# Performance work log

Hardware: AMD Instinct MI355X
Metric: run time of the kernel (lower is better)

The kernel has to match this reference:

```python
import jax, jax.numpy as jnp
import numpy as np

N = 100000      # num_nodes
FEAT = 256      # num_features
H = 128         # hidden
C = 40          # num_classes
K = 4           # hops
RWS = 10        # random-walk samples per node
NL = 2          # nlayer
ALPHA = 0.1


def setup_inputs() -> dict:
    key = jax.random.key(0)
    ks = jax.random.split(key, 10)
    x = jax.random.normal(ks[0], (N, FEAT), dtype=jnp.float32)
    degree = jax.random.uniform(ks[1], (N,), minval=1.0, maxval=64.0, dtype=jnp.float32)
    # precomputed random-walk endpoints per layer per hop: [NL, K, N*RWS]
    ends = jax.random.randint(ks[2], (NL, K, N * RWS), 0, N, dtype=jnp.int32)
    # att init: alpha*(1-alpha)^k, last entry (1-alpha)^K, tiled per layer
    a = ALPHA * (1.0 - ALPHA) ** jnp.arange(K + 1, dtype=jnp.float32)
    a = a.at[-1].set((1.0 - ALPHA) ** K)
    att = jnp.tile(a[None, :], (NL, 1))
    def lin(k, fan_in, fan_out):
        s = 1.0 / np.sqrt(fan_in)
        return jax.random.uniform(k, (fan_in, fan_out), minval=-s, maxval=s, dtype=jnp.float32)
    W0 = lin(ks[3], FEAT, H)
    b0 = jnp.zeros((H,), dtype=jnp.float32)
    W1 = lin(ks[4], H, H)
    b1 = jnp.zeros((H,), dtype=jnp.float32)
    W2 = lin(ks[5], H, C)
    b2 = jnp.zeros((C,), dtype=jnp.float32)
    return {"x": x, "degree": degree, "ends": ends, "att": att,
            "W0": W0, "b0": b0, "W1": W1, "b1": b1, "W2": W2, "b2": b2}


def reference(x, degree, ends, att, W0, b0, W1, b1, W2, b2):
    Ws = [(W0, b0), (W1, b1)]
    starts = jnp.repeat(jnp.arange(N), RWS)          # [N*RWS] walk start node ids
    d_sqrt = jnp.sqrt(degree)                        # degree^0.5
    d_isqrt = jax.lax.rsqrt(degree)                  # degree^-0.5
    h = x
    for i in range(NL):
        W, b = Ws[i]
        h = h @ W + b                                # Linear (dropout p=0)
        mask = att[i]                                # [K+1]
        agg = h * mask[0]
        for k in range(1, K + 1):
            e = ends[i, k - 1]                       # [N*RWS] hop-k endpoints
            w = d_sqrt[starts] * d_isqrt[e]          # degree reweighting
            samp = (w[:, None] * h[e]).reshape(N, RWS, h.shape[1]).mean(axis=1)
            agg = agg + samp * mask[k]
        h = jax.nn.relu(agg)
    logits = h @ W2 + b2
    return jax.nn.log_softmax(logits, axis=1)
```

## Files before the change

kernel.cpp:

```cpp
#include <hip/hip_runtime.h>
#include <math.h>

#define NNODES 100000
#define NFEAT  256
#define HID    128
#define NCLS   40
#define KHOP   4
#define RWSAMP 10
#define KP1    5

typedef __bf16 bf16;
typedef __attribute__((ext_vector_type(8)))  __bf16 bf16x8;
typedef __attribute__((ext_vector_type(2)))  float  f32x2;
typedef __attribute__((ext_vector_type(16))) float  f32x16;

__global__ __launch_bounds__(256) void prep_w(
    const float* __restrict__ W0, const float* __restrict__ W1,
    const float* __restrict__ W2,
    bf16* __restrict__ Wt0, bf16* __restrict__ Wt1, bf16* __restrict__ Wt2)
{
    int tid = blockIdx.x * 256 + threadIdx.x;
    if (tid < 128 * 256) {
        int n = tid >> 8, k = tid & 255;
        Wt0[tid] = (bf16)W0[k * 128 + n];
    } else if (tid < 128 * 256 + 128 * 128) {
        int i = tid - 128 * 256;
        int n = i >> 7, k = i & 127;
        Wt1[i] = (bf16)W1[k * 128 + n];
    } else if (tid < 128 * 256 + 128 * 128 + 64 * 128) {
        int i = tid - (128 * 256 + 128 * 128);
        int n = i >> 7, k = i & 127;
        Wt2[i] = (n < NCLS) ? (bf16)W2[k * NCLS + n] : (bf16)0.0f;
    }
}

template<int K, bool A_BF16>
__global__ __launch_bounds__(256) void gemm_nodes(
    const void* __restrict__ Av, const bf16* __restrict__ Wt,
    const float* __restrict__ bias, unsigned char* __restrict__ F8, int M)
{
    constexpr int BK  = 128;
    constexpr int LDB = BK + 4;
    __shared__ bf16 Bs[128 * LDB];
    __shared__ bf16 As[4][32 * LDB];

    const int tid  = threadIdx.x;
    const int wv   = tid >> 6;
    const int lane = tid & 63;
    const int l31  = lane & 31;
    const int lhi  = lane >> 5;
    const int blockRow = blockIdx.x * 128;
    const int rowBase  = blockRow + wv * 32;

    const bf16*  Ab = (const bf16*)Av;
    const float* Af = (const float*)Av;

    f32x16 acc[4];
#pragma unroll
    for (int t = 0; t < 4; ++t)
#pragma unroll
        for (int r = 0; r < 16; ++r) acc[t][r] = 0.0f;

    for (int k0 = 0; k0 < K; k0 += BK) {
        if (k0) __syncthreads();
#pragma unroll 4
        for (int l = 0; l < 8; ++l) {
            int c   = tid + l * 256;
            int row = c >> 4;
            int kc  = (c & 15) * 8;
            uint4 v = *(const uint4*)(Wt + (size_t)row * K + k0 + kc);
            *(uint2*)&Bs[row * LDB + kc]     = make_uint2(v.x, v.y);
            *(uint2*)&Bs[row * LDB + kc + 4] = make_uint2(v.z, v.w);
        }
        __syncthreads();

        if (A_BF16) {
#pragma unroll 4
            for (int l = 0; l < 8; ++l) {
                int c  = lane + l * 64;
                int r  = c >> 4;
                int kc = (c & 15) * 8;
                int gr = min(rowBase + r, M - 1);
                uint4 v = *(const uint4*)(Ab + (size_t)gr * K + k0 + kc);
                *(uint2*)&As[wv][r * LDB + kc]     = make_uint2(v.x, v.y);
                *(uint2*)&As[wv][r * LDB + kc + 4] = make_uint2(v.z, v.w);
            }
        } else {
#pragma unroll 4
            for (int l = 0; l < 16; ++l) {
                int c  = lane + l * 64;
                int r  = c >> 5;
                int kc = (c & 31) * 4;
                int gr = min(rowBase + r, M - 1);
                float4 v = *(const float4*)(Af + (size_t)gr * K + k0 + kc);
                union { bf16 h[4]; uint2 u; } t4;
                t4.h[0] = (bf16)v.x; t4.h[1] = (bf16)v.y;
                t4.h[2] = (bf16)v.z; t4.h[3] = (bf16)v.w;
                *(uint2*)&As[wv][r * LDB + kc] = t4.u;
            }
        }

#pragma unroll
        for (int ks = 0; ks < BK / 16; ++ks) {
            const int ko = ks * 16 + lhi * 8;
            union { uint2 u2[2]; bf16x8 v; } ua, ub;
            ua.u2[0] = *(const uint2*)&As[wv][l31 * LDB + ko];
            ua.u2[1] = *(const uint2*)&As[wv][l31 * LDB + ko + 4];
            bf16x8 a = ua.v;
#pragma unroll
            for (int t = 0; t < 4; ++t) {
                ub.u2[0] = *(const uint2*)&Bs[(t * 32 + l31) * LDB + ko];
                ub.u2[1] = *(const uint2*)&Bs[(t * 32 + l31) * LDB + ko + 4];
                acc[t] = __builtin_amdgcn_mfma_f32_32x32x16_bf16(a, ub.v, acc[t], 0, 0, 0);
            }
        }
    }

    __syncthreads();
    unsigned* ldsq = (unsigned*)Bs;

#pragma unroll
    for (int t = 0; t < 4; ++t) {
        int col = t * 32 + l31;
        float bc = bias[col];
#pragma unroll
        for (int G = 0; G < 4; ++G) {
            float v0 = acc[t][4 * G + 0] + bc;
            float v1 = acc[t][4 * G + 1] + bc;
            float v2 = acc[t][4 * G + 2] + bc;
            float v3 = acc[t][4 * G + 3] + bc;
            int p = __builtin_amdgcn_cvt_pk_fp8_f32(v0, v1, 0, false);
            p = __builtin_amdgcn_cvt_pk_fp8_f32(v2, v3, p, true);
            ldsq[(wv * 8 + 2 * G + lhi) * 128 + col] = (unsigned)p;
        }
    }
    __syncthreads();

    {
        const int j  = tid & 31;
        const int Q0 = (tid >> 5) * 4;
#pragma unroll
        for (int qq = 0; qq < 4; ++qq) {
            int Q = Q0 + qq;
            uint4 d = *(const uint4*)&ldsq[Q * 128 + 4 * j];
            int growb = blockRow + 4 * Q;
#pragma unroll
            for (int i = 0; i < 4; ++i) {
                unsigned sel = ((unsigned)(4 + i) << 8) | (unsigned)i;
                unsigned lo = __builtin_amdgcn_perm(d.y, d.x, sel);
                unsigned hi = __builtin_amdgcn_perm(d.w, d.z, sel);
                unsigned o  = __builtin_amdgcn_perm(hi, lo, 0x05040100u);
                if (growb + i < M)
                    *(unsigned*)(F8 + (size_t)(growb + i) * 128 + 4 * j) = o;
            }
        }
    }
}

__global__ __launch_bounds__(256) void agg_relu_fp8(
    const unsigned char* __restrict__ hf8, bf16* __restrict__ hout,
    const int* __restrict__ ends, const float* __restrict__ degree,
    const float* __restrict__ att)
{
    __shared__ int2 sew[4][2][40];

    const int wv   = threadIdx.x >> 6;
    const int lane = threadIdx.x & 63;
    const int n0   = blockIdx.x * 8 + wv * 2;

    for (int en = lane; en < 80; en += 64) {
        int which = en >= 40;
        int l = en - which * 40;
        int n = n0 + which;
        int k = l / RWSAMP, s = l - k * RWSAMP;
        int e = ends[(size_t)k * (NNODES * RWSAMP) + (size_t)n * RWSAMP + s];
        float w = att[k + 1] * (1.0f / RWSAMP) * sqrtf(degree[n]) * rsqrtf(degree[e]);
        sew[wv][which][l] = make_int2(e << 7, __float_as_int(w));
    }

    const int q  = lane >> 4;
    const int c8 = (lane & 15) * 8;

    f32x2 a0[4], a1[4];
#pragma unroll
    for (int i = 0; i < 4; ++i) { a0[i] = (f32x2){0.f, 0.f}; a1[i] = (f32x2){0.f, 0.f}; }

#pragma unroll
    for (int t = 0; t < 10; ++t) {
        int2 ew0 = sew[wv][0][4 * t + q];
        int2 ew1 = sew[wv][1][4 * t + q];
        uint2 g0 = *(const uint2*)(hf8 + (unsigned)ew0.x + (unsigned)c8);
        uint2 g1 = *(const uint2*)(hf8 + (unsigned)ew1.x + (unsigned)c8);
        float w0 = __int_as_float(ew0.y);
        float w1 = __int_as_float(ew1.y);
        f32x2 w20 = {w0, w0}, w21 = {w1, w1};
        a0[0] = __builtin_elementwise_fma(w20, __builtin_amdgcn_cvt_pk_f32_fp8((int)g0.x, false), a0[0]);
        a0[1] = __builtin_elementwise_fma(w20, __builtin_amdgcn_cvt_pk_f32_fp8((int)g0.x, true),  a0[1]);
        a0[2] = __builtin_elementwise_fma(w20, __builtin_amdgcn_cvt_pk_f32_fp8((int)g0.y, false), a0[2]);
        a0[3] = __builtin_elementwise_fma(w20, __builtin_amdgcn_cvt_pk_f32_fp8((int)g0.y, true),  a0[3]);
        a1[0] = __builtin_elementwise_fma(w21, __builtin_amdgcn_cvt_pk_f32_fp8((int)g1.x, false), a1[0]);
        a1[1] = __builtin_elementwise_fma(w21, __builtin_amdgcn_cvt_pk_f32_fp8((int)g1.x, true),  a1[1]);
        a1[2] = __builtin_elementwise_fma(w21, __builtin_amdgcn_cvt_pk_f32_fp8((int)g1.y, false), a1[2]);
        a1[3] = __builtin_elementwise_fma(w21, __builtin_amdgcn_cvt_pk_f32_fp8((int)g1.y, true),  a1[3]);
    }

#pragma unroll
    for (int i = 0; i < 4; ++i) {
        a0[i].x += __shfl_xor(a0[i].x, 16, 64); a0[i].y += __shfl_xor(a0[i].y, 16, 64);
        a1[i].x += __shfl_xor(a1[i].x, 16, 64); a1[i].y += __shfl_xor(a1[i].y, 16, 64);
        a0[i].x += __shfl_xor(a0[i].x, 32, 64); a0[i].y += __shfl_xor(a0[i].y, 32, 64);
        a1[i].x += __shfl_xor(a1[i].x, 32, 64); a1[i].y += __shfl_xor(a1[i].y, 32, 64);
    }

    if (q < 2) {
        const int n = n0 + q;
        f32x2* a = (q == 0) ? a0 : a1;
        const float att0 = att[0];
        f32x2 av = {att0, att0};
        unsigned vs = ((unsigned)n << 7) + (unsigned)c8;
        uint2 sv = *(const uint2*)(hf8 + vs);
        a[0] = __builtin_elementwise_fma(av, __builtin_amdgcn_cvt_pk_f32_fp8((int)sv.x, false), a[0]);
        a[1] = __builtin_elementwise_fma(av, __builtin_amdgcn_cvt_pk_f32_fp8((int)sv.x, true),  a[1]);
        a[2] = __builtin_elementwise_fma(av, __builtin_amdgcn_cvt_pk_f32_fp8((int)sv.y, false), a[2]);
        a[3] = __builtin_elementwise_fma(av, __builtin_amdgcn_cvt_pk_f32_fp8((int)sv.y, true),  a[3]);

        f32x2 z = {0.f, 0.f};
#pragma unroll
        for (int i = 0; i < 4; ++i) a[i] = __builtin_elementwise_max(a[i], z);

        union { bf16 h[8]; uint4 u; } st;
        st.h[0] = (bf16)a[0].x; st.h[1] = (bf16)a[0].y;
        st.h[2] = (bf16)a[1].x; st.h[3] = (bf16)a[1].y;
        st.h[4] = (bf16)a[2].x; st.h[5] = (bf16)a[2].y;
        st.h[6] = (bf16)a[3].x; st.h[7] = (bf16)a[3].y;
        *(uint4*)(hout + (size_t)n * HID + c8) = st.u;
    }
}

__global__ __launch_bounds__(256) void head_mfma(
    const bf16* __restrict__ h, const bf16* __restrict__ Wt2,
    const float* __restrict__ b2, float* __restrict__ out, int M)
{
    constexpr int K = HID, LDB = K + 8;
    __shared__ bf16 Bs[64 * LDB];

    const int tid = threadIdx.x;
    constexpr int CPR = K / 8;
    for (int f = tid; f < 64 * CPR; f += 256) {
        int row = f / CPR;
        int kc  = (f % CPR) * 8;
        *(uint4*)&Bs[row * LDB + kc] = *(const uint4*)(Wt2 + (size_t)row * K + kc);
    }
    __syncthreads();

    const int wv   = tid >> 6;
    const int lane = tid & 63;
    const int l31  = lane & 31;
    const int lhi  = lane >> 5;
    const int blockRow = blockIdx.x * 128;
    const int arow = min(blockRow + wv * 32 + l31, M - 1);

    f32x16 acc[2];
#pragma unroll
    for (int t = 0; t < 2; ++t)
#pragma unroll
        for (int r = 0; r < 16; ++r) acc[t][r] = 0.0f;

#pragma unroll
    for (int ks = 0; ks < K / 16; ++ks) {
        bf16x8 a = *(const bf16x8*)(h + (size_t)arow * K + ks * 16 + lhi * 8);
#pragma unroll
        for (int t = 0; t < 2; ++t) {
            bf16x8 b = *(const bf16x8*)&Bs[(t * 32 + l31) * LDB + ks * 16 + lhi * 8];
            acc[t] = __builtin_amdgcn_mfma_f32_32x32x16_bf16(a, b, acc[t], 0, 0, 0);
        }
    }

    const float bc0 = b2[l31];
    const float bc1 = (l31 < 8) ? b2[32 + l31] : 0.0f;

#pragma unroll
    for (int r = 0; r < 16; ++r) {
        float v0 = acc[0][r] + bc0;
        float v1 = (l31 < 8) ? (acc[1][r] + bc1) : -INFINITY;

        float m = fmaxf(v0, v1);
#pragma unroll
        for (int off = 16; off > 0; off >>= 1)
            m = fmaxf(m, __shfl_xor(m, off, 64));

        float s = __expf(v0 - m) + ((l31 < 8) ? __expf(v1 - m) : 0.0f);
#pragma unroll
        for (int off = 16; off > 0; off >>= 1)
            s += __shfl_xor(s, off, 64);

        float ls = __logf(s);
        int grow = blockRow + wv * 32 + (r & 3) + 8 * (r >> 2) + 4 * lhi;
        if (grow < M) {
            out[(size_t)grow * NCLS + l31] = v0 - m - ls;
            if (l31 < 8)
                out[(size_t)grow * NCLS + 32 + l31] = v1 - m - ls;
        }
    }
}

extern "C" void kernel_launch(void* const* d_in, const int* in_sizes, int n_in,
                              void* d_out, int out_size, void* d_ws, size_t ws_size,
                              hipStream_t stream)
{
    const float* x      = (const float*)d_in[0];
    const float* degree = (const float*)d_in[1];
    const int*   ends   = (const int*)  d_in[2];
    const float* att    = (const float*)d_in[3];
    const float* W0     = (const float*)d_in[4];
    const float* b0     = (const float*)d_in[5];
    const float* W1     = (const float*)d_in[6];
    const float* b1     = (const float*)d_in[7];
    const float* W2     = (const float*)d_in[8];
    const float* b2     = (const float*)d_in[9];
    float* out = (float*)d_out;

    bf16* hb0 = (bf16*)d_ws;
    bf16* hb1 = hb0 + (size_t)NNODES * HID;
    unsigned char* hf8 = (unsigned char*)(hb1 + (size_t)NNODES * HID);
    bf16* Wt0 = (bf16*)(hf8 + (size_t)NNODES * HID);
    bf16* Wt1 = Wt0 + 128 * 256;
    bf16* Wt2 = Wt1 + 128 * 128;

    const int prepN = 128 * 256 + 128 * 128 + 64 * 128;
    prep_w<<<(prepN + 255) / 256, 256, 0, stream>>>(W0, W1, W2, Wt0, Wt1, Wt2);

    const int gGemm = (NNODES + 127) / 128;
    const int gAgg  = (NNODES + 7) / 8;

    gemm_nodes<NFEAT, false><<<gGemm, 256, 0, stream>>>(x, Wt0, b0, hf8, NNODES);
    agg_relu_fp8<<<gAgg, 256, 0, stream>>>(hf8, hb1, ends, degree, att);
    gemm_nodes<HID, true><<<gGemm, 256, 0, stream>>>(hb1, Wt1, b1, hf8, NNODES);
    agg_relu_fp8<<<gAgg, 256, 0, stream>>>(
        hf8, hb0, ends + (size_t)KHOP * NNODES * RWSAMP, degree, att + KP1);
    head_mfma<<<gGemm, 256, 0, stream>>>(hb0, Wt2, b2, out, NNODES);
}
```

Baseline: 350.6 us.

## Stage gathered fp8 neighbor rows into LDS via global_load_lds before aggregation

The aggregation kernel now issues all 82 row gathers per wave (40 walk endpoints per node plus the self row, for two nodes) as direct global-to-LDS loads into a per-wave staging buffer, waits once, then reads the rows from LDS for the FMA reduction. Endpoint offsets and weights are split into separate LDS arrays, and the self term is folded into the same staged rows. The intent is to expose more gathers in flight at once and to avoid register-held global loads. In exchange it uses about 42KB of LDS per block, which may reduce occupancy. It also adds a full vmcnt wait with no overlap between loading and compute.

```diff
diff --git a/kernel.cpp b/kernel.cpp
--- a/kernel.cpp
+++ b/kernel.cpp
@@ -13,6 +13,9 @@
 typedef __attribute__((ext_vector_type(8)))  __bf16 bf16x8;
 typedef __attribute__((ext_vector_type(2)))  float  f32x2;
 typedef __attribute__((ext_vector_type(16))) float  f32x16;
+
+typedef __attribute__((address_space(3))) unsigned       lds_u32;
+typedef __attribute__((address_space(1))) const unsigned glb_u32;
 
 __global__ __launch_bounds__(256) void prep_w(
     const float* __restrict__ W0, const float* __restrict__ W1,
@@ -162,21 +165,46 @@
     const int* __restrict__ ends, const float* __restrict__ degree,
     const float* __restrict__ att)
 {
-    __shared__ int2 sew[4][2][40];
+    __shared__ __attribute__((aligned(16))) unsigned char stage[4][82 * 128];
+    __shared__ int   sewE[4][82];
+    __shared__ float sewW[4][82];
 
     const int wv   = threadIdx.x >> 6;
     const int lane = threadIdx.x & 63;
     const int n0   = blockIdx.x * 8 + wv * 2;
 
-    for (int en = lane; en < 80; en += 64) {
-        int which = en >= 40;
-        int l = en - which * 40;
-        int n = n0 + which;
-        int k = l / RWSAMP, s = l - k * RWSAMP;
-        int e = ends[(size_t)k * (NNODES * RWSAMP) + (size_t)n * RWSAMP + s];
-        float w = att[k + 1] * (1.0f / RWSAMP) * sqrtf(degree[n]) * rsqrtf(degree[e]);
-        sew[wv][which][l] = make_int2(e << 7, __float_as_int(w));
-    }
+    for (int en = lane; en < 82; en += 64) {
+        int node = en > 40;
+        int j = en - node * 41;
+        int n = n0 + node;
+        int e;
+        float w;
+        if (j == 40) {
+            e = n;
+            w = att[0];
+        } else {
+            int k = j / RWSAMP, s = j - k * RWSAMP;
+            e = ends[(size_t)k * (NNODES * RWSAMP) + (size_t)n * RWSAMP + s];
+            w = att[k + 1] * (1.0f / RWSAMP) * sqrtf(degree[n]) * rsqrtf(degree[e]);
+        }
+        sewE[wv][en] = e << 7;
+        sewW[wv][en] = w;
+    }
+
+    {
+        const unsigned char* gbase = hf8 + (unsigned)((lane & 31) * 4);
+#pragma unroll
+        for (int t = 0; t < 41; ++t) {
+            int r = 2 * t + (lane >> 5);
+            int eoff = sewE[wv][r];
+            __builtin_amdgcn_global_load_lds(
+                (glb_u32*)(gbase + (unsigned)eoff),
+                (lds_u32*)&stage[wv][t * 256],
+                4, 0, 0);
+        }
+    }
+    asm volatile("s_waitcnt vmcnt(0)" ::: "memory");
+    __builtin_amdgcn_sched_barrier(0);
 
     const int q  = lane >> 4;
     const int c8 = (lane & 15) * 8;
@@ -187,12 +215,11 @@
 
 #pragma unroll
     for (int t = 0; t < 10; ++t) {
-        int2 ew0 = sew[wv][0][4 * t + q];
-        int2 ew1 = sew[wv][1][4 * t + q];
-        uint2 g0 = *(const uint2*)(hf8 + (unsigned)ew0.x + (unsigned)c8);
-        uint2 g1 = *(const uint2*)(hf8 + (unsigned)ew1.x + (unsigned)c8);
-        float w0 = __int_as_float(ew0.y);
-        float w1 = __int_as_float(ew1.y);
+        int j = 4 * t + q;
+        uint2 g0 = *(const uint2*)&stage[wv][j * 128 + c8];
+        uint2 g1 = *(const uint2*)&stage[wv][(41 + j) * 128 + c8];
+        float w0 = sewW[wv][j];
+        float w1 = sewW[wv][41 + j];
         f32x2 w20 = {w0, w0}, w21 = {w1, w1};
         a0[0] = __builtin_elementwise_fma(w20, __builtin_amdgcn_cvt_pk_f32_fp8((int)g0.x, false), a0[0]);
         a0[1] = __builtin_elementwise_fma(w20, __builtin_amdgcn_cvt_pk_f32_fp8((int)g0.x, true),  a0[1]);
@@ -215,10 +242,10 @@
     if (q < 2) {
         const int n = n0 + q;
         f32x2* a = (q == 0) ? a0 : a1;
-        const float att0 = att[0];
+        const int selfRow = q ? 81 : 40;
+        uint2 sv = *(const uint2*)&stage[wv][selfRow * 128 + c8];
+        float att0 = sewW[wv][selfRow];
         f32x2 av = {att0, att0};
-        unsigned vs = ((unsigned)n << 7) + (unsigned)c8;
-        uint2 sv = *(const uint2*)(hf8 + vs);
         a[0] = __builtin_elementwise_fma(av, __builtin_amdgcn_cvt_pk_f32_fp8((int)sv.x, false), a[0]);
         a[1] = __builtin_elementwise_fma(av, __builtin_amdgcn_cvt_pk_f32_fp8((int)sv.x, true),  a[1]);
         a[2] = __builtin_elementwise_fma(av, __builtin_amdgcn_cvt_pk_f32_fp8((int)sv.y, false), a[2]);
```

Result: slower. 393.9 us (+12.4%).

## Fold degree scaling into GEMM epilogue and restructure aggregation to one node per wave

Applied to the files above, without the earlier changes.

The GEMM epilogue now multiplies each row by rsqrt(degree) before FP8 quantisation. The aggregation therefore no longer gathers degree[e] for every random-walk endpoint and applies sqrt(degree[n]) once, after ReLU. The aggregation kernel is also rebuilt so each wave handles one node with 16-byte gathers, 8 lanes per row and a one-step software prefetch. The self term is handled as a 41st sample slot. Pre-scaling values before FP8 changes their dynamic range, which may affect quantisation error slightly.

```diff
diff --git a/kernel.cpp b/kernel.cpp
--- a/kernel.cpp
+++ b/kernel.cpp
@@ -37,7 +37,8 @@
 template<int K, bool A_BF16>
 __global__ __launch_bounds__(256) void gemm_nodes(
     const void* __restrict__ Av, const bf16* __restrict__ Wt,
-    const float* __restrict__ bias, unsigned char* __restrict__ F8, int M)
+    const float* __restrict__ bias, const float* __restrict__ degree,
+    unsigned char* __restrict__ F8, int M)
 {
     constexpr int BK  = 128;
     constexpr int LDB = BK + 4;
@@ -116,6 +117,15 @@
         }
     }
 
+    float rsd[16];
+#pragma unroll
+    for (int G = 0; G < 4; ++G) {
+        int r0 = blockRow + 4 * (wv * 8 + 2 * G + lhi);
+#pragma unroll
+        for (int c = 0; c < 4; ++c)
+            rsd[4 * G + c] = rsqrtf(degree[min(r0 + c, M - 1)]);
+    }
+
     __syncthreads();
     unsigned* ldsq = (unsigned*)Bs;
 
@@ -125,10 +135,10 @@
         float bc = bias[col];
 #pragma unroll
         for (int G = 0; G < 4; ++G) {
-            float v0 = acc[t][4 * G + 0] + bc;
-            float v1 = acc[t][4 * G + 1] + bc;
-            float v2 = acc[t][4 * G + 2] + bc;
-            float v3 = acc[t][4 * G + 3] + bc;
+            float v0 = (acc[t][4 * G + 0] + bc) * rsd[4 * G + 0];
+            float v1 = (acc[t][4 * G + 1] + bc) * rsd[4 * G + 1];
+            float v2 = (acc[t][4 * G + 2] + bc) * rsd[4 * G + 2];
+            float v3 = (acc[t][4 * G + 3] + bc) * rsd[4 * G + 3];
             int p = __builtin_amdgcn_cvt_pk_fp8_f32(v0, v1, 0, false);
             p = __builtin_amdgcn_cvt_pk_fp8_f32(v2, v3, p, true);
             ldsq[(wv * 8 + 2 * G + lhi) * 128 + col] = (unsigned)p;
@@ -162,78 +172,88 @@
     const int* __restrict__ ends, const float* __restrict__ degree,
     const float* __restrict__ att)
 {
-    __shared__ int2 sew[4][2][40];
+    __shared__ int   sewE[4][48];
+    __shared__ float sewW[4][48];
 
     const int wv   = threadIdx.x >> 6;
     const int lane = threadIdx.x & 63;
-    const int n0   = blockIdx.x * 8 + wv * 2;
-
-    for (int en = lane; en < 80; en += 64) {
-        int which = en >= 40;
-        int l = en - which * 40;
-        int n = n0 + which;
-        int k = l / RWSAMP, s = l - k * RWSAMP;
-        int e = ends[(size_t)k * (NNODES * RWSAMP) + (size_t)n * RWSAMP + s];
-        float w = att[k + 1] * (1.0f / RWSAMP) * sqrtf(degree[n]) * rsqrtf(degree[e]);
-        sew[wv][which][l] = make_int2(e << 7, __float_as_int(w));
-    }
-
-    const int q  = lane >> 4;
-    const int c8 = (lane & 15) * 8;
-
-    f32x2 a0[4], a1[4];
-#pragma unroll
-    for (int i = 0; i < 4; ++i) { a0[i] = (f32x2){0.f, 0.f}; a1[i] = (f32x2){0.f, 0.f}; }
-
-#pragma unroll
-    for (int t = 0; t < 10; ++t) {
-        int2 ew0 = sew[wv][0][4 * t + q];
-        int2 ew1 = sew[wv][1][4 * t + q];
-        uint2 g0 = *(const uint2*)(hf8 + (unsigned)ew0.x + (unsigned)c8);
-        uint2 g1 = *(const uint2*)(hf8 + (unsigned)ew1.x + (unsigned)c8);
-        float w0 = __int_as_float(ew0.y);
-        float w1 = __int_as_float(ew1.y);
-        f32x2 w20 = {w0, w0}, w21 = {w1, w1};
-        a0[0] = __builtin_elementwise_fma(w20, __builtin_amdgcn_cvt_pk_f32_fp8((int)g0.x, false), a0[0]);
-        a0[1] = __builtin_elementwise_fma(w20, __builtin_amdgcn_cvt_pk_f32_fp8((int)g0.x, true),  a0[1]);
-        a0[2] = __builtin_elementwise_fma(w20, __builtin_amdgcn_cvt_pk_f32_fp8((int)g0.y, false), a0[2]);
-        a0[3] = __builtin_elementwise_fma(w20, __builtin_amdgcn_cvt_pk_f32_fp8((int)g0.y, true),  a0[3]);
-        a1[0] = __builtin_elementwise_fma(w21, __builtin_amdgcn_cvt_pk_f32_fp8((int)g1.x, false), a1[0]);
-        a1[1] = __builtin_elementwise_fma(w21, __builtin_amdgcn_cvt_pk_f32_fp8((int)g1.x, true),  a1[1]);
-        a1[2] = __builtin_elementwise_fma(w21, __builtin_amdgcn_cvt_pk_f32_fp8((int)g1.y, false), a1[2]);
-        a1[3] = __builtin_elementwise_fma(w21, __builtin_amdgcn_cvt_pk_f32_fp8((int)g1.y, true),  a1[3]);
-    }
-
-#pragma unroll
-    for (int i = 0; i < 4; ++i) {
-        a0[i].x += __shfl_xor(a0[i].x, 16, 64); a0[i].y += __shfl_xor(a0[i].y, 16, 64);
-        a1[i].x += __shfl_xor(a1[i].x, 16, 64); a1[i].y += __shfl_xor(a1[i].y, 16, 64);
-        a0[i].x += __shfl_xor(a0[i].x, 32, 64); a0[i].y += __shfl_xor(a0[i].y, 32, 64);
-        a1[i].x += __shfl_xor(a1[i].x, 32, 64); a1[i].y += __shfl_xor(a1[i].y, 32, 64);
-    }
-
-    if (q < 2) {
-        const int n = n0 + q;
-        f32x2* a = (q == 0) ? a0 : a1;
-        const float att0 = att[0];
-        f32x2 av = {att0, att0};
-        unsigned vs = ((unsigned)n << 7) + (unsigned)c8;
-        uint2 sv = *(const uint2*)(hf8 + vs);
-        a[0] = __builtin_elementwise_fma(av, __builtin_amdgcn_cvt_pk_f32_fp8((int)sv.x, false), a[0]);
-        a[1] = __builtin_elementwise_fma(av, __builtin_amdgcn_cvt_pk_f32_fp8((int)sv.x, true),  a[1]);
-        a[2] = __builtin_elementwise_fma(av, __builtin_amdgcn_cvt_pk_f32_fp8((int)sv.y, false), a[2]);
-        a[3] = __builtin_elementwise_fma(av, __builtin_amdgcn_cvt_pk_f32_fp8((int)sv.y, true),  a[3]);
-
-        f32x2 z = {0.f, 0.f};
-#pragma unroll
-        for (int i = 0; i < 4; ++i) a[i] = __builtin_elementwise_max(a[i], z);
-
-        union { bf16 h[8]; uint4 u; } st;
-        st.h[0] = (bf16)a[0].x; st.h[1] = (bf16)a[0].y;
-        st.h[2] = (bf16)a[1].x; st.h[3] = (bf16)a[1].y;
-        st.h[4] = (bf16)a[2].x; st.h[5] = (bf16)a[2].y;
-        st.h[6] = (bf16)a[3].x; st.h[7] = (bf16)a[3].y;
-        *(uint4*)(hout + (size_t)n * HID + c8) = st.u;
+    const int n    = blockIdx.x * 4 + wv;
+
+    if (lane < 48) {
+        int j = lane;
+        int e; float w;
+        if (j < 40) {
+            int k = j / RWSAMP, ss = j - k * RWSAMP;
+            e = ends[(size_t)k * (NNODES * RWSAMP) + (size_t)n * RWSAMP + ss];
+            w = att[k + 1] * (1.0f / RWSAMP);
+        } else if (j == 40) { e = n; w = att[0]; }
+        else                { e = n; w = 0.0f;  }
+        sewE[wv][j] = e << 7;
+        sewW[wv][j] = w;
+    }
+
+    const int s  = lane >> 3;
+    const int fc = lane & 7;
+
+    int   eoff[6];
+    float wt[6];
+#pragma unroll
+    for (int t = 0; t < 6; ++t) {
+        eoff[t] = sewE[wv][8 * t + s];
+        wt[t]   = sewW[wv][8 * t + s];
+    }
+
+    const unsigned char* base = hf8 + (unsigned)(fc * 16);
+    uint4 cur = *(const uint4*)(base + (unsigned)eoff[0]);
+
+    f32x2 acc[8];
+#pragma unroll
+    for (int i = 0; i < 8; ++i) acc[i] = (f32x2){0.f, 0.f};
+
+#pragma unroll
+    for (int t = 0; t < 6; ++t) {
+        uint4 nxt = cur;
+        if (t < 5) nxt = *(const uint4*)(base + (unsigned)eoff[t + 1]);
+        float w = wt[t];
+        f32x2 w2 = {w, w};
+        acc[0] = __builtin_elementwise_fma(w2, __builtin_amdgcn_cvt_pk_f32_fp8((int)cur.x, false), acc[0]);
+        acc[1] = __builtin_elementwise_fma(w2, __builtin_amdgcn_cvt_pk_f32_fp8((int)cur.x, true),  acc[1]);
+        acc[2] = __builtin_elementwise_fma(w2, __builtin_amdgcn_cvt_pk_f32_fp8((int)cur.y, false), acc[2]);
+        acc[3] = __builtin_elementwise_fma(w2, __builtin_amdgcn_cvt_pk_f32_fp8((int)cur.y, true),  acc[3]);
+        acc[4] = __builtin_elementwise_fma(w2, __builtin_amdgcn_cvt_pk_f32_fp8((int)cur.z, false), acc[4]);
+        acc[5] = __builtin_elementwise_fma(w2, __builtin_amdgcn_cvt_pk_f32_fp8((int)cur.z, true),  acc[5]);
+        acc[6] = __builtin_elementwise_fma(w2, __builtin_amdgcn_cvt_pk_f32_fp8((int)cur.w, false), acc[6]);
+        acc[7] = __builtin_elementwise_fma(w2, __builtin_amdgcn_cvt_pk_f32_fp8((int)cur.w, true),  acc[7]);
+        cur = nxt;
+    }
+
+#pragma unroll
+    for (int i = 0; i < 8; ++i) {
+        acc[i].x += __shfl_xor(acc[i].x, 8, 64);  acc[i].y += __shfl_xor(acc[i].y, 8, 64);
+        acc[i].x += __shfl_xor(acc[i].x, 16, 64); acc[i].y += __shfl_xor(acc[i].y, 16, 64);
+        acc[i].x += __shfl_xor(acc[i].x, 32, 64); acc[i].y += __shfl_xor(acc[i].y, 32, 64);
+    }
+
+    if (s == 0) {
+        float sd = sqrtf(degree[n]);
+        f32x2 sd2 = {sd, sd}, z = {0.f, 0.f};
+#pragma unroll
+        for (int i = 0; i < 8; ++i) {
+            acc[i] = __builtin_elementwise_max(acc[i], z);
+            acc[i] = acc[i] * sd2;
+        }
+        union { bf16 h[8]; uint4 u; } lo, hi;
+        lo.h[0] = (bf16)acc[0].x; lo.h[1] = (bf16)acc[0].y;
+        lo.h[2] = (bf16)acc[1].x; lo.h[3] = (bf16)acc[1].y;
+        lo.h[4] = (bf16)acc[2].x; lo.h[5] = (bf16)acc[2].y;
+        lo.h[6] = (bf16)acc[3].x; lo.h[7] = (bf16)acc[3].y;
+        hi.h[0] = (bf16)acc[4].x; hi.h[1] = (bf16)acc[4].y;
+        hi.h[2] = (bf16)acc[5].x; hi.h[3] = (bf16)acc[5].y;
+        hi.h[4] = (bf16)acc[6].x; hi.h[5] = (bf16)acc[6].y;
+        hi.h[6] = (bf16)acc[7].x; hi.h[7] = (bf16)acc[7].y;
+        bf16* orow = hout + (size_t)n * HID + fc * 16;
+        *(uint4*)orow       = lo.u;
+        *(uint4*)(orow + 8) = hi.u;
     }
 }
 
@@ -331,11 +351,11 @@
     prep_w<<<(prepN + 255) / 256, 256, 0, stream>>>(W0, W1, W2, Wt0, Wt1, Wt2);
 
     const int gGemm = (NNODES + 127) / 128;
-    const int gAgg  = (NNODES + 7) / 8;
-
-    gemm_nodes<NFEAT, false><<<gGemm, 256, 0, stream>>>(x, Wt0, b0, hf8, NNODES);
+    const int gAgg  = NNODES / 4;
+
+    gemm_nodes<NFEAT, false><<<gGemm, 256, 0, stream>>>(x, Wt0, b0, degree, hf8, NNODES);
     agg_relu_fp8<<<gAgg, 256, 0, stream>>>(hf8, hb1, ends, degree, att);
-    gemm_nodes<HID, true><<<gGemm, 256, 0, stream>>>(hb1, Wt1, b1, hf8, NNODES);
+    gemm_nodes<HID, true><<<gGemm, 256, 0, stream>>>(hb1, Wt1, b1, degree, hf8, NNODES);
     agg_relu_fp8<<<gAgg, 256, 0, stream>>>(
         hf8, hb0, ends + (size_t)KHOP * NNODES * RWSAMP, degree, att + KP1);
     head_mfma<<<gGemm, 256, 0, stream>>>(hb0, Wt2, b2, out, NNODES);
```

After: 358.9 us. 1.02x slower.

## Fold degree reweighting into GEMM epilogue and drop per-endpoint degree gathers

Applied to the files above, without the earlier changes.

The GEMM epilogue now scales each node's features by rsqrt(degree) before the fp8 pack. The aggregation kernel then multiplies by sqrt(degree[n]) after the ReLU, which is valid because the scale is positive. This removes a random gather of degree[e] for every walk endpoint. Per-hop weights move into a small shared table, and the self term joins the gather loop as an eleventh iteration. The cost is an added block-wide barrier and a change in fp8 quantisation, since the stored values are now pre-scaled.

```diff
diff --git a/kernel.cpp b/kernel.cpp
--- a/kernel.cpp
+++ b/kernel.cpp
@@ -37,7 +37,8 @@
 template<int K, bool A_BF16>
 __global__ __launch_bounds__(256) void gemm_nodes(
     const void* __restrict__ Av, const bf16* __restrict__ Wt,
-    const float* __restrict__ bias, unsigned char* __restrict__ F8, int M)
+    const float* __restrict__ bias, const float* __restrict__ degree,
+    unsigned char* __restrict__ F8, int M)
 {
     constexpr int BK  = 128;
     constexpr int LDB = BK + 4;
@@ -116,6 +117,15 @@
         }
     }
 
+    float rsd[16];
+#pragma unroll
+    for (int G = 0; G < 4; ++G) {
+        int r0 = blockRow + 4 * (wv * 8 + 2 * G + lhi);
+#pragma unroll
+        for (int c = 0; c < 4; ++c)
+            rsd[4 * G + c] = rsqrtf(degree[min(r0 + c, M - 1)]);
+    }
+
     __syncthreads();
     unsigned* ldsq = (unsigned*)Bs;
 
@@ -125,10 +135,10 @@
         float bc = bias[col];
 #pragma unroll
         for (int G = 0; G < 4; ++G) {
-            float v0 = acc[t][4 * G + 0] + bc;
-            float v1 = acc[t][4 * G + 1] + bc;
-            float v2 = acc[t][4 * G + 2] + bc;
-            float v3 = acc[t][4 * G + 3] + bc;
+            float v0 = (acc[t][4 * G + 0] + bc) * rsd[4 * G + 0];
+            float v1 = (acc[t][4 * G + 1] + bc) * rsd[4 * G + 1];
+            float v2 = (acc[t][4 * G + 2] + bc) * rsd[4 * G + 2];
+            float v3 = (acc[t][4 * G + 3] + bc) * rsd[4 * G + 3];
             int p = __builtin_amdgcn_cvt_pk_fp8_f32(v0, v1, 0, false);
             p = __builtin_amdgcn_cvt_pk_fp8_f32(v2, v3, p, true);
             ldsq[(wv * 8 + 2 * G + lhi) * 128 + col] = (unsigned)p;
@@ -162,11 +172,21 @@
     const int* __restrict__ ends, const float* __restrict__ degree,
     const float* __restrict__ att)
 {
-    __shared__ int2 sew[4][2][40];
+    __shared__ int   sewE[4][2][40];
+    __shared__ float sw[44];
 
     const int wv   = threadIdx.x >> 6;
     const int lane = threadIdx.x & 63;
     const int n0   = blockIdx.x * 8 + wv * 2;
+
+    if (threadIdx.x < 44) {
+        int j = threadIdx.x;
+        float w;
+        if (j < 40)       w = att[j / RWSAMP + 1] * (1.0f / RWSAMP);
+        else if (j == 40) w = att[0];
+        else              w = 0.0f;
+        sw[j] = w;
+    }
 
     for (int en = lane; en < 80; en += 64) {
         int which = en >= 40;
@@ -174,9 +194,9 @@
         int n = n0 + which;
         int k = l / RWSAMP, s = l - k * RWSAMP;
         int e = ends[(size_t)k * (NNODES * RWSAMP) + (size_t)n * RWSAMP + s];
-        float w = att[k + 1] * (1.0f / RWSAMP) * sqrtf(degree[n]) * rsqrtf(degree[e]);
-        sew[wv][which][l] = make_int2(e << 7, __float_as_int(w));
-    }
+        sewE[wv][which][l] = e << 7;
+    }
+    __syncthreads();
 
     const int q  = lane >> 4;
     const int c8 = (lane & 15) * 8;
@@ -186,22 +206,23 @@
     for (int i = 0; i < 4; ++i) { a0[i] = (f32x2){0.f, 0.f}; a1[i] = (f32x2){0.f, 0.f}; }
 
 #pragma unroll
-    for (int t = 0; t < 10; ++t) {
-        int2 ew0 = sew[wv][0][4 * t + q];
-        int2 ew1 = sew[wv][1][4 * t + q];
-        uint2 g0 = *(const uint2*)(hf8 + (unsigned)ew0.x + (unsigned)c8);
-        uint2 g1 = *(const uint2*)(hf8 + (unsigned)ew1.x + (unsigned)c8);
-        float w0 = __int_as_float(ew0.y);
-        float w1 = __int_as_float(ew1.y);
-        f32x2 w20 = {w0, w0}, w21 = {w1, w1};
-        a0[0] = __builtin_elementwise_fma(w20, __builtin_amdgcn_cvt_pk_f32_fp8((int)g0.x, false), a0[0]);
-        a0[1] = __builtin_elementwise_fma(w20, __builtin_amdgcn_cvt_pk_f32_fp8((int)g0.x, true),  a0[1]);
-        a0[2] = __builtin_elementwise_fma(w20, __builtin_amdgcn_cvt_pk_f32_fp8((int)g0.y, false), a0[2]);
-        a0[3] = __builtin_elementwise_fma(w20, __builtin_amdgcn_cvt_pk_f32_fp8((int)g0.y, true),  a0[3]);
-        a1[0] = __builtin_elementwise_fma(w21, __builtin_amdgcn_cvt_pk_f32_fp8((int)g1.x, false), a1[0]);
-        a1[1] = __builtin_elementwise_fma(w21, __builtin_amdgcn_cvt_pk_f32_fp8((int)g1.x, true),  a1[1]);
-        a1[2] = __builtin_elementwise_fma(w21, __builtin_amdgcn_cvt_pk_f32_fp8((int)g1.y, false), a1[2]);
-        a1[3] = __builtin_elementwise_fma(w21, __builtin_amdgcn_cvt_pk_f32_fp8((int)g1.y, true),  a1[3]);
+    for (int t = 0; t < 11; ++t) {
+        int j = 4 * t + q;
+        int e0, e1;
+        if (t < 10) { e0 = sewE[wv][0][j]; e1 = sewE[wv][1][j]; }
+        else        { e0 = n0 << 7;        e1 = (n0 + 1) << 7; }
+        float w = sw[j];
+        uint2 g0 = *(const uint2*)(hf8 + (unsigned)e0 + (unsigned)c8);
+        uint2 g1 = *(const uint2*)(hf8 + (unsigned)e1 + (unsigned)c8);
+        f32x2 w2 = {w, w};
+        a0[0] = __builtin_elementwise_fma(w2, __builtin_amdgcn_cvt_pk_f32_fp8((int)g0.x, false), a0[0]);
+        a0[1] = __builtin_elementwise_fma(w2, __builtin_amdgcn_cvt_pk_f32_fp8((int)g0.x, true),  a0[1]);
+        a0[2] = __builtin_elementwise_fma(w2, __builtin_amdgcn_cvt_pk_f32_fp8((int)g0.y, false), a0[2]);
+        a0[3] = __builtin_elementwise_fma(w2, __builtin_amdgcn_cvt_pk_f32_fp8((int)g0.y, true),  a0[3]);
+        a1[0] = __builtin_elementwise_fma(w2, __builtin_amdgcn_cvt_pk_f32_fp8((int)g1.x, false), a1[0]);
+        a1[1] = __builtin_elementwise_fma(w2, __builtin_amdgcn_cvt_pk_f32_fp8((int)g1.x, true),  a1[1]);
+        a1[2] = __builtin_elementwise_fma(w2, __builtin_amdgcn_cvt_pk_f32_fp8((int)g1.y, false), a1[2]);
+        a1[3] = __builtin_elementwise_fma(w2, __builtin_amdgcn_cvt_pk_f32_fp8((int)g1.y, true),  a1[3]);
     }
 
 #pragma unroll
@@ -215,18 +236,13 @@
     if (q < 2) {
         const int n = n0 + q;
         f32x2* a = (q == 0) ? a0 : a1;
-        const float att0 = att[0];
-        f32x2 av = {att0, att0};
-        unsigned vs = ((unsigned)n << 7) + (unsigned)c8;
-        uint2 sv = *(const uint2*)(hf8 + vs);
-        a[0] = __builtin_elementwise_fma(av, __builtin_amdgcn_cvt_pk_f32_fp8((int)sv.x, false), a[0]);
-        a[1] = __builtin_elementwise_fma(av, __builtin_amdgcn_cvt_pk_f32_fp8((int)sv.x, true),  a[1]);
-        a[2] = __builtin_elementwise_fma(av, __builtin_amdgcn_cvt_pk_f32_fp8((int)sv.y, false), a[2]);
-        a[3] = __builtin_elementwise_fma(av, __builtin_amdgcn_cvt_pk_f32_fp8((int)sv.y, true),  a[3]);
-
-        f32x2 z = {0.f, 0.f};
-#pragma unroll
-        for (int i = 0; i < 4; ++i) a[i] = __builtin_elementwise_max(a[i], z);
+        float sd = sqrtf(degree[n]);
+        f32x2 sd2 = {sd, sd}, z = {0.f, 0.f};
+#pragma unroll
+        for (int i = 0; i < 4; ++i) {
+            a[i] = __builtin_elementwise_max(a[i], z);
+            a[i] = a[i] * sd2;
+        }
 
         union { bf16 h[8]; uint4 u; } st;
         st.h[0] = (bf16)a[0].x; st.h[1] = (bf16)a[0].y;
@@ -333,9 +349,9 @@
     const int gGemm = (NNODES + 127) / 128;
     const int gAgg  = (NNODES + 7) / 8;
 
-    gemm_nodes<NFEAT, false><<<gGemm, 256, 0, stream>>>(x, Wt0, b0, hf8, NNODES);
+    gemm_nodes<NFEAT, false><<<gGemm, 256, 0, stream>>>(x, Wt0, b0, degree, hf8, NNODES);
     agg_relu_fp8<<<gAgg, 256, 0, stream>>>(hf8, hb1, ends, degree, att);
-    gemm_nodes<HID, true><<<gGemm, 256, 0, stream>>>(hb1, Wt1, b1, hf8, NNODES);
+    gemm_nodes<HID, true><<<gGemm, 256, 0, stream>>>(hb1, Wt1, b1, degree, hf8, NNODES);
     agg_relu_fp8<<<gAgg, 256, 0, stream>>>(
         hf8, hb0, ends + (size_t)KHOP * NNODES * RWSAMP, degree, att + KP1);
     head_mfma<<<gGemm, 256, 0, stream>>>(hb0, Wt2, b2, out, NNODES);
```

Measured after the change: 334.7 us (median of 2 runs). 1.05x faster.
